# Performance work log

Measured on AMD Instinct MI355X. Metric: run time of the kernel, lower is better.

Reference implementation:

```python
import jax, jax.numpy as jnp
import numpy as np


def _bilinear_zeros(yb, ix, iy):
    # yb: [C,H,W]; ix, iy: [D,H,W] pixel coords (align_corners=False convention)
    # zeros padding: each corner masked individually, matching F.grid_sample
    h, w = yb.shape[1], yb.shape[2]
    x0 = jnp.floor(ix)
    y0 = jnp.floor(iy)
    wx = ix - x0  # [D,H,W]
    wy = iy - y0
    x0i = x0.astype(jnp.int32)
    y0i = y0.astype(jnp.int32)
    x1i = x0i + 1
    y1i = y0i + 1

    def gather(yi, xi):
        m = ((xi >= 0) & (xi < w) & (yi >= 0) & (yi < h)).astype(yb.dtype)
        yc = jnp.clip(yi, 0, h - 1)
        xc = jnp.clip(xi, 0, w - 1)
        return yb[:, yc, xc] * m[None]  # [C,D,H,W]

    v00 = gather(y0i, x0i)
    v01 = gather(y0i, x1i)
    v10 = gather(y1i, x0i)
    v11 = gather(y1i, x1i)
    wx = wx[None]
    wy = wy[None]
    return (v00 * (1 - wx) * (1 - wy) + v01 * wx * (1 - wy)
            + v10 * (1 - wx) * wy + v11 * wx * wy)


def cost_volume(x, y, disp_range_samples, ndisp):
    bs, c, h, w = x.shape
    dt = x.dtype
    mw = jnp.arange(w, dtype=dt)  # [W]
    mh = jnp.arange(h, dtype=dt)  # [H]
    # normalized grid coords as in the torch module (align_corners=True style normalize)
    cur_x = mw[None, None, None, :] - disp_range_samples  # [B,D,H,W]
    gx = cur_x / ((w - 1.0) / 2.0) - 1.0
    gy = mh / ((h - 1.0) / 2.0) - 1.0  # [H]
    # F.grid_sample default align_corners=False unnormalization
    ix = ((gx + 1.0) * w - 1.0) * 0.5  # [B,D,H,W]
    iy = ((gy + 1.0) * h - 1.0) * 0.5  # [H]
    iy_full = jnp.broadcast_to(iy[None, None, :, None], ix.shape)
    warped = jax.vmap(_bilinear_zeros)(y, ix, iy_full)  # [B,C,D,H,W]
    left = jnp.broadcast_to(x[:, :, None, :, :], (bs, c, ndisp, h, w))
    return jnp.concatenate([left, warped], axis=1)  # [B,2C,D,H,W]


def setup_inputs() -> dict:
    key = jax.random.key(0)
    k1, k2, k3 = jax.random.split(key, 3)
    B, C, H, W, D = 1, 32, 128, 256, 48
    x = jax.random.normal(k1, (B, C, H, W), dtype=jnp.float32)
    y = jax.random.normal(k2, (B, C, H, W), dtype=jnp.float32)
    disp = jax.random.uniform(k3, (B, D, H, W), dtype=jnp.float32) * 64.0
    return {"x": x, "y": y, "disp_range_samples": disp, "ndisp": D}


def reference(x, y, disp_range_samples, ndisp):
    return cost_volume(x, y, disp_range_samples, ndisp)
```

## Files before the change

### kernel.cpp

```cpp
#include <hip/hip_runtime.h>


typedef float v4f __attribute__((ext_vector_type(4)));

namespace {
constexpr int C = 32, D = 48, H = 128, W = 256;
constexpr int HW  = H * W;
constexpr int DHW = D * HW;
constexpr int SPAN = 324;
constexpr int XLO  = -66;
constexpr int CP   = 20;
}

__global__ __launch_bounds__(512, 4) void cost_volume_kernel(
    const float* __restrict__ x, const float* __restrict__ y,
    const float* __restrict__ disp, float* __restrict__ out)
{
    __shared__ __align__(16) float ys[2 * SPAN * CP];

    const int t     = threadIdx.x;
    const int bx    = blockIdx.x;
    const int h     = bx >> 2;
    const int ch    = (bx >> 1) & 1;
    const int dh    = bx & 1;
    const int cb    = ch * 16;
    const int dbase = dh * 24;

    const float gy  = (float)h / 63.5f - 1.0f;
    const float iy  = ((gy + 1.0f) * 128.0f - 1.0f) * 0.5f;
    const float y0f = floorf(iy);
    const float wy  = iy - y0f;
    const int   y0i = (int)y0f;

    {
        const int combo = t >> 4;
        const int row = combo >> 4;
        const int cc  = combo & 15;
        const int yr  = y0i + row;
        const bool vr = (yr >= 0) && (yr < H);
        const float* ysrc = y + (cb + cc) * HW + yr * W;
        for (int j = (t & 15); j < SPAN; j += 16) {
            const int xg = XLO + j;
            float v = 0.0f;
            if (vr && xg >= 0 && xg < W) v = ysrc[xg];
            ys[(row * SPAN + j) * CP + cc] = v;
        }
    }

    const int wave = t >> 6;
    const int lane = t & 63;
    const int w0   = 4 * lane;

    v4f xv0 = *(const v4f*)(x + (cb + wave * 2 + 0) * HW + h * W + w0);
    v4f xv1 = *(const v4f*)(x + (cb + wave * 2 + 1) * HW + h * W + w0);

    __syncthreads();

    const float omy = 1.0f - wy;
    float* const outw = out + (C + cb) * DHW + h * W + w0;

    for (int dd = 0; dd < 3; ++dd) {
        const int d = dbase + wave * 3 + dd;
        const v4f dv = *(const v4f*)(disp + d * HW + h * W + w0);
        float wgt[4][4]; int jj[4];
#pragma unroll
        for (int k = 0; k < 4; ++k) {
            const float cur = (float)(w0 + k) - dv[k];
            const float gx  = cur / 127.5f - 1.0f;
            const float ix  = ((gx + 1.0f) * 256.0f - 1.0f) * 0.5f;
            const float x0f = floorf(ix);
            const float wx  = ix - x0f;
            jj[k] = min(max((int)x0f - XLO, 0), SPAN - 2);
            const float omx = 1.0f - wx;
            wgt[k][0] = omx * omy; wgt[k][1] = wx * omy;
            wgt[k][2] = omx * wy;  wgt[k][3] = wx * wy;
        }
#pragma unroll
        for (int cq = 0; cq < 4; ++cq) {
            const int c0 = cq * 4;
            float res[4][4];
#pragma unroll
            for (int k = 0; k < 4; ++k) {
                const float* p0 = ys + jj[k] * CP + c0;
                const float* p1 = p0 + SPAN * CP;
                const v4f v00 = *(const v4f*)p0;
                const v4f v01 = *(const v4f*)(p0 + CP);
                const v4f v10 = *(const v4f*)p1;
                const v4f v11 = *(const v4f*)(p1 + CP);
#pragma unroll
                for (int cc = 0; cc < 4; ++cc)
                    res[cc][k] = fmaf(v11[cc], wgt[k][3], fmaf(v10[cc], wgt[k][2],
                                  fmaf(v01[cc], wgt[k][1], v00[cc] * wgt[k][0])));
            }
#pragma unroll
            for (int cc = 0; cc < 4; ++cc) {
                const v4f r = { res[cc][0], res[cc][1], res[cc][2], res[cc][3] };
                *(v4f*)(outw + (c0 + cc) * DHW + d * HW) = r;
            }
        }
    }

    {
        float* op0 = out + (cb + wave * 2 + 0) * DHW + dbase * HW + h * W + w0;
        float* op1 = out + (cb + wave * 2 + 1) * DHW + dbase * HW + h * W + w0;
        for (int d = 0; d < 24; ++d) {
            *(v4f*)(op0 + d * HW) = xv0;
            *(v4f*)(op1 + d * HW) = xv1;
        }
    }
}

extern "C" void kernel_launch(void* const* d_in, const int* in_sizes, int n_in,
                              void* d_out, int out_size, void* d_ws, size_t ws_size,
                              hipStream_t stream) {
    const float* x    = (const float*)d_in[0];
    const float* y    = (const float*)d_in[1];
    const float* disp = (const float*)d_in[2];
    float* out = (float*)d_out;

    cost_volume_kernel<<<dim3(512), dim3(512), 0, stream>>>(x, y, disp, out);
}
```

Before: 415.6 us.

## Retile cost volume kernel per channel with row strips and scalar LDS gathers

Changes the block decomposition from (row, channel-half, disparity-half) to (channel, 8-disparity group, 32-row strip). Each block stages a 34-row window of a single channel of y in padded shared memory and loops over 32 rows per wave. The old layout read channel-interleaved float4 vectors from shared memory; the new one does scalar gathers per corner. The aim is to cut redundant staging of y and per-block overhead, but it loses the vectorized 16-channel reuse of the computed weights and index math. The disparity index math is now recomputed once per channel instead of being shared across 16 channels.

```diff
diff --git a/kernel.cpp b/kernel.cpp
--- a/kernel.cpp
+++ b/kernel.cpp
@@ -9,60 +9,63 @@
 constexpr int DHW = D * HW;
 constexpr int SPAN = 324;
 constexpr int XLO  = -66;
-constexpr int CP   = 20;
+constexpr int ROWS = 34;
+constexpr int SP   = SPAN + 1;
 }
 
 __global__ __launch_bounds__(512, 4) void cost_volume_kernel(
     const float* __restrict__ x, const float* __restrict__ y,
     const float* __restrict__ disp, float* __restrict__ out)
 {
-    __shared__ __align__(16) float ys[2 * SPAN * CP];
+    __shared__ float ys[ROWS * SP];
 
     const int t     = threadIdx.x;
-    const int bx    = blockIdx.x;
-    const int h     = bx >> 2;
-    const int ch    = (bx >> 1) & 1;
-    const int dh    = bx & 1;
-    const int cb    = ch * 16;
-    const int dbase = dh * 24;
+    const int c     = blockIdx.x;
+    const int dbase = blockIdx.y * 8;
+    const int h0    = blockIdx.z * 32;
+    const int wave  = t >> 6;
+    const int lane  = t & 63;
+    const int w0    = 4 * lane;
 
-    const float gy  = (float)h / 63.5f - 1.0f;
-    const float iy  = ((gy + 1.0f) * 128.0f - 1.0f) * 0.5f;
-    const float y0f = floorf(iy);
-    const float wy  = iy - y0f;
-    const int   y0i = (int)y0f;
+    v4f xv[4];
+#pragma unroll
+    for (int q = 0; q < 4; ++q)
+        xv[q] = *(const v4f*)(x + c * HW + (h0 + wave * 4 + q) * W + w0);
 
-    {
-        const int combo = t >> 4;
-        const int row = combo >> 4;
-        const int cc  = combo & 15;
-        const int yr  = y0i + row;
-        const bool vr = (yr >= 0) && (yr < H);
-        const float* ysrc = y + (cb + cc) * HW + yr * W;
-        for (int j = (t & 15); j < SPAN; j += 16) {
-            const int xg = XLO + j;
-            float v = 0.0f;
-            if (vr && xg >= 0 && xg < W) v = ysrc[xg];
-            ys[(row * SPAN + j) * CP + cc] = v;
-        }
+    const float gy0 = (float)h0 / 63.5f - 1.0f;
+    const float iy0 = ((gy0 + 1.0f) * 128.0f - 1.0f) * 0.5f;
+    const int   rlo = (int)floorf(iy0);
+
+    const float* ysrc = y + c * HW;
+    for (int i = t; i < ROWS * SPAN; i += 512) {
+        const int r  = i / SPAN;
+        const int j  = i - r * SPAN;
+        const int yr = rlo + r;
+        const int xg = XLO + j;
+        float v = 0.0f;
+        if (yr >= 0 && yr < H && xg >= 0 && xg < W) v = ysrc[yr * W + xg];
+        ys[r * SP + j] = v;
     }
-
-    const int wave = t >> 6;
-    const int lane = t & 63;
-    const int w0   = 4 * lane;
-
-    v4f xv0 = *(const v4f*)(x + (cb + wave * 2 + 0) * HW + h * W + w0);
-    v4f xv1 = *(const v4f*)(x + (cb + wave * 2 + 1) * HW + h * W + w0);
-
     __syncthreads();
 
-    const float omy = 1.0f - wy;
-    float* const outw = out + (C + cb) * DHW + h * W + w0;
+    const int d = dbase + wave;
+    const float* dp   = disp + d * HW + h0 * W + w0;
+    float*       wout = out + (C + c) * DHW + d * HW + h0 * W + w0;
 
-    for (int dd = 0; dd < 3; ++dd) {
-        const int d = dbase + wave * 3 + dd;
-        const v4f dv = *(const v4f*)(disp + d * HW + h * W + w0);
-        float wgt[4][4]; int jj[4];
+    for (int hh = 0; hh < 32; ++hh) {
+        const int h = h0 + hh;
+        const v4f dv = *(const v4f*)(dp + hh * W);
+
+        const float gyh = (float)h / 63.5f - 1.0f;
+        const float iyh = ((gyh + 1.0f) * 128.0f - 1.0f) * 0.5f;
+        const float y0f = floorf(iyh);
+        const float wy  = iyh - y0f;
+        const float omy = 1.0f - wy;
+        const int   r0  = (int)y0f - rlo;
+        const float* row0 = ys + r0 * SP;
+        const float* row1 = row0 + SP;
+
+        float res[4];
 #pragma unroll
         for (int k = 0; k < 4; ++k) {
             const float cur = (float)(w0 + k) - dv[k];
@@ -70,43 +73,25 @@
             const float ix  = ((gx + 1.0f) * 256.0f - 1.0f) * 0.5f;
             const float x0f = floorf(ix);
             const float wx  = ix - x0f;
-            jj[k] = min(max((int)x0f - XLO, 0), SPAN - 2);
+            const int j = min(max((int)x0f - XLO, 0), SPAN - 2);
             const float omx = 1.0f - wx;
-            wgt[k][0] = omx * omy; wgt[k][1] = wx * omy;
-            wgt[k][2] = omx * wy;  wgt[k][3] = wx * wy;
+            const float w00 = omx * omy, w01 = wx * omy;
+            const float w10 = omx * wy,  w11 = wx * wy;
+            const float v00 = row0[j], v01 = row0[j + 1];
+            const float v10 = row1[j], v11 = row1[j + 1];
+            res[k] = fmaf(v11, w11, fmaf(v10, w10,
+                      fmaf(v01, w01, v00 * w00)));
         }
-#pragma unroll
-        for (int cq = 0; cq < 4; ++cq) {
-            const int c0 = cq * 4;
-            float res[4][4];
-#pragma unroll
-            for (int k = 0; k < 4; ++k) {
-                const float* p0 = ys + jj[k] * CP + c0;
-                const float* p1 = p0 + SPAN * CP;
-                const v4f v00 = *(const v4f*)p0;
-                const v4f v01 = *(const v4f*)(p0 + CP);
-                const v4f v10 = *(const v4f*)p1;
-                const v4f v11 = *(const v4f*)(p1 + CP);
-#pragma unroll
-                for (int cc = 0; cc < 4; ++cc)
-                    res[cc][k] = fmaf(v11[cc], wgt[k][3], fmaf(v10[cc], wgt[k][2],
-                                  fmaf(v01[cc], wgt[k][1], v00[cc] * wgt[k][0])));
-            }
-#pragma unroll
-            for (int cc = 0; cc < 4; ++cc) {
-                const v4f r = { res[cc][0], res[cc][1], res[cc][2], res[cc][3] };
-                *(v4f*)(outw + (c0 + cc) * DHW + d * HW) = r;
-            }
-        }
+        const v4f r = { res[0], res[1], res[2], res[3] };
+        *(v4f*)(wout + hh * W) = r;
     }
 
-    {
-        float* op0 = out + (cb + wave * 2 + 0) * DHW + dbase * HW + h * W + w0;
-        float* op1 = out + (cb + wave * 2 + 1) * DHW + dbase * HW + h * W + w0;
-        for (int d = 0; d < 24; ++d) {
-            *(v4f*)(op0 + d * HW) = xv0;
-            *(v4f*)(op1 + d * HW) = xv1;
-        }
+#pragma unroll
+    for (int dd = 0; dd < 8; ++dd) {
+        float* lp = out + c * DHW + (dbase + dd) * HW + (h0 + wave * 4) * W + w0;
+#pragma unroll
+        for (int q = 0; q < 4; ++q)
+            *(v4f*)(lp + q * W) = xv[q];
     }
 }
 
@@ -118,5 +103,5 @@
     const float* disp = (const float*)d_in[2];
     float* out = (float*)d_out;
 
-    cost_volume_kernel<<<dim3(512), dim3(512), 0, stream>>>(x, y, disp, out);
+    cost_volume_kernel<<<dim3(32, 6, 4), dim3(512), 0, stream>>>(x, y, disp, out);
 }
```

New measurement: 433.5 us. +4.3%, slower.
